# Kernel optimization log

Measured on AMD Instinct MI355X. Metric: run time of the kernel, lower is better.

Reference implementation:

```python
import jax, jax.numpy as jnp
import numpy as np

B, H, W, E = 8, 64, 64, 256  # channels == embedding (required by final Multiply)


def setup_inputs() -> dict:
    key = jax.random.key(0)
    k1, k2, k3 = jax.random.split(key, 3)
    inputs = jax.random.normal(k1, (B, H, W, E), dtype=jnp.float32)
    # Conv2D(embedding, 3, padding='same') params, HWIO layout
    conv_w = jax.random.normal(k2, (3, 3, E, E), dtype=jnp.float32) * (1.0 / np.sqrt(9 * E))
    conv_b = jnp.zeros((E,), dtype=jnp.float32)
    return {"inputs": inputs, "conv_w": conv_w, "conv_b": conv_b}


def reference(inputs, conv_w, conv_b):
    emb = conv_w.shape[-1]
    # conv1: 3x3 same-padded conv, NHWC
    x = jax.lax.conv_general_dilated(
        inputs, conv_w, window_strides=(1, 1), padding="SAME",
        dimension_numbers=("NHWC", "HWIO", "NHWC")) + conv_b
    b, h, w, e = x.shape
    x1 = x.reshape(b, h * w, e)                       # [B, N, E]
    scores = jnp.einsum("bne,bme->bnm", x1, x1)       # [B, N, N]
    attn = jax.nn.softmax(scores, axis=-1) / jnp.sqrt(jnp.asarray(emb, x.dtype))
    out = jnp.einsum("bnm,bme->bne", attn, x1)        # [B, N, E]
    # Original keras uses Reshape((inputs.shape[-2], inputs.shape[-3], -1)): (W, H, E)
    out = out.reshape(b, w, h, e)
    return out * inputs
```

## Files before the change

### kernel.cpp

```cpp
#include <hip/hip_runtime.h>
#include <hip/hip_bf16.h>

typedef __attribute__((ext_vector_type(4))) float f32x4;
typedef __attribute__((ext_vector_type(8))) _Float16 f16x8;
typedef unsigned short u16;

#define NB 8
#define NE 256
#define NN 4096
#define SD 64

__device__ __forceinline__ void gload_lds16(const void* g, void* l) {
  __builtin_amdgcn_global_load_lds((const __attribute__((address_space(1))) void*)g,
                                   (__attribute__((address_space(3))) void*)l, 16, 0, 0);
}
__device__ __forceinline__ float fexp2(float x) {
#if __has_builtin(__builtin_amdgcn_exp2f)
  return __builtin_amdgcn_exp2f(x);
#else
  return exp2f(x);
#endif
}

__global__ __launch_bounds__(256) void k_prep(const float* __restrict__ x, u16* __restrict__ outF,
                                              const float* __restrict__ w, u16* __restrict__ wT) {
  int bid = blockIdx.x;
  int tid = threadIdx.x;
  if (bid < 8192) {
    int i = bid * 256 + tid;
    float4 v = reinterpret_cast<const float4*>(x)[i];
    ushort4 o;
    o.x = __builtin_bit_cast(u16, (_Float16)v.x);
    o.y = __builtin_bit_cast(u16, (_Float16)v.y);
    o.z = __builtin_bit_cast(u16, (_Float16)v.z);
    o.w = __builtin_bit_cast(u16, (_Float16)v.w);
    reinterpret_cast<ushort4*>(outF)[i] = o;
  } else {
    int i = (bid - 8192) * 256 + tid;
    int t = i >> 16;
    int r = i & 65535;
    int ei = r >> 8, eo = r & 255;
    int o = (t << 16) + (eo << 8) + ei;
    wT[o] = __builtin_bit_cast(u16, (_Float16)w[i]);
  }
}

__global__ __launch_bounds__(256, 2) void k_conv(const u16* __restrict__ inF,
                                                 const u16* __restrict__ wT,
                                                 const float* __restrict__ bias,
                                                 u16* __restrict__ x1h) {
  __shared__ u16 Ahalo[264 * 64];
  __shared__ u16 BhL[2][128 * 64];
  int b = blockIdx.x >> 6;
  int rem = blockIdx.x & 63;
  int mt = rem >> 1, et = rem & 1;
  int h0 = mt << 1;
  int tid = threadIdx.x;
  int wid = tid >> 6, lane = tid & 63;
  int wr = wid >> 1, wc = wid & 1;
  int r = lane & 15, g = lane >> 4;
  f32x4 acc[4][4];
#pragma unroll
  for (int i = 0; i < 4; ++i)
#pragma unroll
    for (int j = 0; j < 4; ++j) acc[i][j] = (f32x4){0.f, 0.f, 0.f, 0.f};
  const long ibase = (long)b * NN * NE;

  const int bsw = ((((lane & 7) << 4) ^ (((lane >> 3) & 7) << 4)) >> 1);
  long bSrc[4];
#pragma unroll
  for (int i = 0; i < 4; ++i) {
    int c = wid * 4 + i;
    int eo = c * 8 + (lane >> 3);
    bSrc[i] = (long)(et * 128 + eo) * 256 + bsw;
  }
  int aHalo[9];
  const u16* aSrc[9];
#pragma unroll
  for (int j = 0; j < 9; ++j) {
    int c = wid + 4 * j;
    int slot = c * 8 + (lane >> 3);
    int hr = slot >= 198 ? 3 : (slot >= 132 ? 2 : (slot >= 66 ? 1 : 0));
    int hc = slot - hr * 66;
    int ir = h0 - 1 + hr, ic = hc - 1;
    aHalo[j] = ((unsigned)ir >= 64u) | ((unsigned)ic >= 64u);
    int irc = min(max(ir, 0), 63), icc = min(max(ic, 0), 63);
    int c8s = (lane & 7) ^ (slot & 7);
    aSrc[j] = inF + ibase + ((long)(irc * 64 + icc) << 8) + c8s * 8;
  }

#pragma unroll
  for (int i = 0; i < 4; ++i)
    gload_lds16(wT + bSrc[i], (char*)BhL[0] + (wid * 4 + i) * 1024);

#pragma unroll 1
  for (int kc = 0; kc < 4; ++kc) {
    __builtin_amdgcn_s_barrier();
#pragma unroll
    for (int j = 0; j < 9; ++j) {
      int c = wid + 4 * j;
      if (c < 33)
        gload_lds16(aSrc[j] + kc * 64, (char*)Ahalo + c * 1024);
    }
    asm volatile("s_waitcnt vmcnt(0)" ::: "memory");
#pragma unroll
    for (int j = 0; j < 9; ++j) {
      int c = wid + 4 * j;
      if (c < 33 && aHalo[j])
        *reinterpret_cast<float4*>((char*)Ahalo + c * 1024 + (lane << 4)) =
            make_float4(0.f, 0.f, 0.f, 0.f);
    }
    asm volatile("s_waitcnt lgkmcnt(0)" ::: "memory");
    __builtin_amdgcn_s_barrier();

#pragma unroll 1
    for (int t = 0; t < 9; ++t) {
      int gidx = kc * 9 + t;
      if (t > 0) {
        asm volatile("s_waitcnt vmcnt(0)" ::: "memory");
        __builtin_amdgcn_s_barrier();
      }
      if (gidx < 35) {
        int nt = t + 1 == 9 ? 0 : t + 1;
        int nkc = t + 1 == 9 ? kc + 1 : kc;
        long tkoff = ((long)nt << 16) + nkc * 64;
        char* dstB = (char*)BhL[(gidx + 1) & 1];
#pragma unroll
        for (int i = 0; i < 4; ++i)
          gload_lds16(wT + tkoff + bSrc[i], dstB + (wid * 4 + i) * 1024);
      }
      const u16* BB = BhL[gidx & 1];
      int dy = t / 3 - 1, dx = t % 3 - 1;
      int abase = (wr + 1 + dy) * 66 + 1 + dx;
#pragma unroll
      for (int ks = 0; ks < 2; ++ks) {
        int c8 = ks * 4 + g;
        f16x8 ah[4], bh[4];
#pragma unroll
        for (int mi = 0; mi < 4; ++mi) {
          int slot = abase + mi * 16 + r;
          int abyte = (slot << 7) + ((c8 << 4) ^ ((slot & 7) << 4));
          ah[mi] = *reinterpret_cast<const f16x8*>(reinterpret_cast<const char*>(Ahalo) + abyte);
        }
#pragma unroll
        for (int ni = 0; ni < 4; ++ni) {
          int col = wc * 64 + ni * 16 + r;
          int bbyte = (col << 7) + ((c8 << 4) ^ ((r & 7) << 4));
          bh[ni] = *reinterpret_cast<const f16x8*>(reinterpret_cast<const char*>(BB) + bbyte);
        }
#pragma unroll
        for (int mi = 0; mi < 4; ++mi)
#pragma unroll
          for (int ni = 0; ni < 4; ++ni)
            acc[mi][ni] = __builtin_amdgcn_mfma_f32_16x16x32_f16(ah[mi], bh[ni], acc[mi][ni], 0, 0, 0);
      }
    }
  }
#pragma unroll
  for (int mi = 0; mi < 4; ++mi)
#pragma unroll
    for (int ni = 0; ni < 4; ++ni) {
      int eo = et * 128 + wc * 64 + ni * 16 + r;
      float bz = bias[eo];
#pragma unroll
      for (int i = 0; i < 4; ++i) {
        int pix = mt * 128 + wr * 64 + mi * 16 + g * 4 + i;
        float v = acc[mi][ni][i] + bz;
        long o = ibase + (long)pix * NE + eo;
        x1h[o] = __builtin_bit_cast(u16, (_Float16)v);
      }
    }
}

__global__ __launch_bounds__(256) void k_trans(const u16* __restrict__ x1h, u16* __restrict__ x1T) {
  __shared__ u16 T[64][72];
  int bid = blockIdx.x;
  int b = bid >> 8, rem = bid & 255;
  int mt = rem >> 2, et = rem & 3;
  int tid = threadIdx.x;
  for (int c = tid; c < 512; c += 256) {
    int rr = c >> 3, c8 = c & 7;
    *reinterpret_cast<float4*>(&T[rr][c8 * 8]) =
        *reinterpret_cast<const float4*>(x1h + ((long)b * NN + mt * 64 + rr) * NE + et * 64 + c8 * 8);
  }
  __syncthreads();
  for (int c = tid; c < 512; c += 256) {
    int er = c >> 3, m8 = c & 7;
    union { u16 u[8]; float4 v; } p;
#pragma unroll
    for (int j = 0; j < 8; ++j) p.u[j] = T[m8 * 8 + j][er];
    *reinterpret_cast<float4*>(x1T + ((long)b * NE + et * 64 + er) * NN + mt * 64 + m8 * 8) = p.v;
  }
}

__global__ __launch_bounds__(256, 3) void k_flash7(const u16* __restrict__ x1h16,
                                                   const u16* __restrict__ x1T,
                                                   const float* __restrict__ inp,
                                                   float* __restrict__ out) {
  __shared__ char LDS[49152];
  int phys = blockIdx.x;
  int b = phys & 7;
  int qt = phys >> 3;
  int tid = threadIdx.x, wid = tid >> 6, lane = tid & 63;
  int l15 = lane & 15, g4 = (lane >> 4) & 3;
  const long bN = (long)b << 12;
  const long vtb = (long)b << 20;

  const long qrow = bN + qt * 64 + wid * 16 + l15;
  f16x8 qh[8];
#pragma unroll
  for (int kc = 0; kc < 8; ++kc) {
    qh[kc] = *reinterpret_cast<const f16x8*>(x1h16 + (qrow << 8) + kc * 32 + g4 * 8);
#pragma unroll
    for (int j = 0; j < 8; ++j)
      qh[kc][j] = (_Float16)((float)qh[kc][j] * 1.44269504f);
  }

  f32x4 o16[16];
#pragma unroll
  for (int et = 0; et < 16; ++et) o16[et] = (f32x4){0.f, 0.f, 0.f, 0.f};
  float mrow = -1.0e30f, lrow = 0.f;

  const u16* kS[4];
  const u16* vS[4];
  int off[4];
#pragma unroll
  for (int i = 0; i < 4; ++i) {
    int c = wid * 4 + i;
    off[i] = c << 10;
    int kr = c * 2 + (lane >> 5);
    int kcolb = ((lane & 31) << 4) ^ ((kr & 15) << 4);
    kS[i] = x1h16 + ((bN + kr) << 8) + (kcolb >> 1);
    int rp = c * 16 + (lane >> 2);
    int e = rp ^ ((rp >> 2) & 1);
    int vcolb = ((lane & 3) << 4) ^ ((e & 3) << 4);
    vS[i] = x1T + vtb + ((long)e << 12) + (vcolb >> 1);
  }

  const int vbase = ((l15 << 6) ^ ((l15 & 4) << 4)) + ((g4 * 16) ^ ((l15 & 3) << 4));
  const int kxor = l15 << 4;
  const int srcA = ((lane >> 4) & 1) * 32 + l15;
  const int srcB = srcA + 16;
  const bool hiHalf = (lane & 32) != 0;

#pragma unroll
  for (int i = 0; i < 4; ++i) { gload_lds16(kS[i], LDS + off[i]); kS[i] += 8192; }

#pragma unroll 1
  for (int it = 0; it < 128; ++it) {
    const char* KB = LDS + (it & 1) * 16384;
    char* VB = LDS + 32768;

    asm volatile("s_waitcnt vmcnt(0)" ::: "memory");
    __builtin_amdgcn_s_barrier();
    __builtin_amdgcn_sched_barrier(0);

    f32x4 st0 = (f32x4){0.f, 0.f, 0.f, 0.f}, st1 = st0;
    int krow0 = l15 << 9, krow1 = (16 + l15) << 9;
    __builtin_amdgcn_s_setprio(1);
#pragma unroll
    for (int kc = 0; kc < 8; ++kc) {
      int kb = (kc * 64 + g4 * 16) ^ kxor;
      f16x8 k0 = *reinterpret_cast<const f16x8*>(KB + krow0 + kb);
      f16x8 k1 = *reinterpret_cast<const f16x8*>(KB + krow1 + kb);
      st0 = __builtin_amdgcn_mfma_f32_16x16x32_f16(k0, qh[kc], st0, 0, 0, 0);
      st1 = __builtin_amdgcn_mfma_f32_16x16x32_f16(k1, qh[kc], st1, 0, 0, 0);
    }
    __builtin_amdgcn_s_setprio(0);

#pragma unroll
    for (int i = 0; i < 4; ++i) { gload_lds16(vS[i], VB + off[i]); vS[i] += 32; }
    if (it < 127) {
      char* KD = LDS + ((it + 1) & 1) * 16384;
#pragma unroll
      for (int i = 0; i < 4; ++i) { gload_lds16(kS[i], KD + off[i]); kS[i] += 8192; }
    }

    float tmax = fmaxf(fmaxf(fmaxf(st0[0], st0[1]), fmaxf(st0[2], st0[3])),
                       fmaxf(fmaxf(st1[0], st1[1]), fmaxf(st1[2], st1[3])));
    tmax = fmaxf(tmax, __shfl_xor(tmax, 16));
    tmax = fmaxf(tmax, __shfl_xor(tmax, 32));
    if (!__all(tmax <= mrow + 11.54f)) {
      float mnew = fmaxf(mrow, tmax);
      float alpha = fexp2(mrow - mnew);
      lrow *= alpha;
      float ar[4];
#pragma unroll
      for (int i = 0; i < 4; ++i) ar[i] = __shfl(alpha, g4 * 4 + i);
#pragma unroll
      for (int et = 0; et < 16; ++et)
#pragma unroll
        for (int i = 0; i < 4; ++i) o16[et][i] *= ar[i];
      mrow = mnew;
    }
#pragma unroll
    for (int i = 0; i < 4; ++i) { st0[i] = fexp2(st0[i] - mrow); st1[i] = fexp2(st1[i] - mrow); }
    float psum = (st0[0] + st0[1]) + (st0[2] + st0[3]) + (st1[0] + st1[1]) + (st1[2] + st1[3]);
    psum += __shfl_xor(psum, 16);
    psum += __shfl_xor(psum, 32);
    lrow += psum;

    int W0, W1, W2, W3;
    {
      unsigned a0 = __builtin_bit_cast(u16, (_Float16)st0[0]);
      unsigned a1 = __builtin_bit_cast(u16, (_Float16)st0[1]);
      unsigned a2 = __builtin_bit_cast(u16, (_Float16)st0[2]);
      unsigned a3 = __builtin_bit_cast(u16, (_Float16)st0[3]);
      unsigned b0 = __builtin_bit_cast(u16, (_Float16)st1[0]);
      unsigned b1 = __builtin_bit_cast(u16, (_Float16)st1[1]);
      unsigned b2 = __builtin_bit_cast(u16, (_Float16)st1[2]);
      unsigned b3 = __builtin_bit_cast(u16, (_Float16)st1[3]);
      W0 = (int)(a0 | (a1 << 16)); W1 = (int)(a2 | (a3 << 16));
      W2 = (int)(b0 | (b1 << 16)); W3 = (int)(b2 | (b3 << 16));
    }
    union PU { int w[4]; f16x8 v; } pa;
    {
      int u0a = __shfl(W0, srcA), u2a = __shfl(W2, srcA);
      int u1a = __shfl(W1, srcA), u3a = __shfl(W3, srcA);
      int u0b = __shfl(W0, srcB), u2b = __shfl(W2, srcB);
      int u1b = __shfl(W1, srcB), u3b = __shfl(W3, srcB);
      pa.w[0] = hiHalf ? u2a : u0a;
      pa.w[1] = hiHalf ? u3a : u1a;
      pa.w[2] = hiHalf ? u2b : u0b;
      pa.w[3] = hiHalf ? u3b : u1b;
    }

    if (it < 127) {
      asm volatile("s_waitcnt vmcnt(4)" ::: "memory");
    } else {
      asm volatile("s_waitcnt vmcnt(0)" ::: "memory");
    }
    __builtin_amdgcn_s_barrier();
    __builtin_amdgcn_sched_barrier(0);

    __builtin_amdgcn_s_setprio(1);
#pragma unroll
    for (int et = 0; et < 16; ++et) {
      f16x8 v = *reinterpret_cast<const f16x8*>(VB + vbase + et * 1024);
      o16[et] = __builtin_amdgcn_mfma_f32_16x16x32_f16(pa.v, v, o16[et], 0, 0, 0);
    }
    __builtin_amdgcn_s_setprio(0);
  }

  float linv = 1.0f / (16.0f * lrow);
  float lr[4];
#pragma unroll
  for (int i = 0; i < 4; ++i) lr[i] = __shfl(linv, g4 * 4 + i);
  const long ob = (bN + qt * 64 + wid * 16) << 8;
#pragma unroll
  for (int et = 0; et < 16; ++et)
#pragma unroll
    for (int i = 0; i < 4; ++i) {
      long off2 = ob + ((long)(g4 * 4 + i) << 8) + et * 16 + l15;
      out[off2] = o16[et][i] * lr[i] * inp[off2];
    }
}

extern "C" void kernel_launch(void* const* d_in, const int* in_sizes, int n_in,
                              void* d_out, int out_size, void* d_ws, size_t ws_size,
                              hipStream_t stream) {
  const float* inp   = (const float*)d_in[0];
  const float* convw = (const float*)d_in[1];
  const float* convb = (const float*)d_in[2];
  float* out = (float*)d_out;
  char* ws = (char*)d_ws;

  u16* x1h = (u16*)(ws);
  u16* x1T = (u16*)(ws + 16777216L);
  u16* inF = (u16*)(ws + 33554432L);
  u16* wT  = (u16*)(ws + 50331648L);

  k_prep<<<10496, 256, 0, stream>>>(inp, inF, convw, wT);
  k_conv<<<512, 256, 0, stream>>>(inF, wT, convb, x1h);
  k_trans<<<2048, 256, 0, stream>>>(x1h, x1T);
  k_flash7<<<512, 256, 0, stream>>>(x1h, x1T, inp, out);
}
```

Measured before the change: 287.6 us.

## Split attention KV range across two blocks and merge partials in separate kernel

The flash-attention kernel now splits each query tile's key/value sequence into two halves handled by separate blocks, doubling the grid from 512 to 1024. Each block writes unnormalized partial outputs plus its row max and row sum to workspace. A new merge kernel combines the halves with log-sum-exp rescaling, normalizes, and applies the final multiply by the inputs. The aim is better CU occupancy and more parallelism, at the cost of extra global traffic for the fp32 partials, an additional kernel launch, and a possible tail wave.

```diff
diff --git a/kernel.cpp b/kernel.cpp
--- a/kernel.cpp
+++ b/kernel.cpp
@@ -193,18 +193,20 @@
   }
 }
 
-__global__ __launch_bounds__(256, 3) void k_flash7(const u16* __restrict__ x1h16,
+__global__ __launch_bounds__(256, 3) void k_flash8(const u16* __restrict__ x1h16,
                                                    const u16* __restrict__ x1T,
-                                                   const float* __restrict__ inp,
-                                                   float* __restrict__ out) {
+                                                   float* __restrict__ Opart,
+                                                   float* __restrict__ ml) {
   __shared__ char LDS[49152];
   int phys = blockIdx.x;
   int b = phys & 7;
-  int qt = phys >> 3;
+  int half = (phys >> 3) & 1;
+  int qt = phys >> 4;
   int tid = threadIdx.x, wid = tid >> 6, lane = tid & 63;
   int l15 = lane & 15, g4 = (lane >> 4) & 3;
   const long bN = (long)b << 12;
   const long vtb = (long)b << 20;
+  const int kv0 = half << 11;
 
   const long qrow = bN + qt * 64 + wid * 16 + l15;
   f16x8 qh[8];
@@ -230,11 +232,11 @@
     off[i] = c << 10;
     int kr = c * 2 + (lane >> 5);
     int kcolb = ((lane & 31) << 4) ^ ((kr & 15) << 4);
-    kS[i] = x1h16 + ((bN + kr) << 8) + (kcolb >> 1);
+    kS[i] = x1h16 + ((bN + kv0 + kr) << 8) + (kcolb >> 1);
     int rp = c * 16 + (lane >> 2);
     int e = rp ^ ((rp >> 2) & 1);
     int vcolb = ((lane & 3) << 4) ^ ((e & 3) << 4);
-    vS[i] = x1T + vtb + ((long)e << 12) + (vcolb >> 1);
+    vS[i] = x1T + vtb + ((long)e << 12) + kv0 + (vcolb >> 1);
   }
 
   const int vbase = ((l15 << 6) ^ ((l15 & 4) << 4)) + ((g4 * 16) ^ ((l15 & 3) << 4));
@@ -247,7 +249,7 @@
   for (int i = 0; i < 4; ++i) { gload_lds16(kS[i], LDS + off[i]); kS[i] += 8192; }
 
 #pragma unroll 1
-  for (int it = 0; it < 128; ++it) {
+  for (int it = 0; it < 64; ++it) {
     const char* KB = LDS + (it & 1) * 16384;
     char* VB = LDS + 32768;
 
@@ -270,7 +272,7 @@
 
 #pragma unroll
     for (int i = 0; i < 4; ++i) { gload_lds16(vS[i], VB + off[i]); vS[i] += 32; }
-    if (it < 127) {
+    if (it < 63) {
       char* KD = LDS + ((it + 1) & 1) * 16384;
 #pragma unroll
       for (int i = 0; i < 4; ++i) { gload_lds16(kS[i], KD + off[i]); kS[i] += 8192; }
@@ -325,7 +327,7 @@
       pa.w[3] = hiHalf ? u3b : u1b;
     }
 
-    if (it < 127) {
+    if (it < 63) {
       asm volatile("s_waitcnt vmcnt(4)" ::: "memory");
     } else {
       asm volatile("s_waitcnt vmcnt(0)" ::: "memory");
@@ -342,18 +344,38 @@
     __builtin_amdgcn_s_setprio(0);
   }
 
-  float linv = 1.0f / (16.0f * lrow);
-  float lr[4];
-#pragma unroll
-  for (int i = 0; i < 4; ++i) lr[i] = __shfl(linv, g4 * 4 + i);
-  const long ob = (bN + qt * 64 + wid * 16) << 8;
+  const long grow0 = bN + qt * 64 + wid * 16;
+  float* Oh = Opart + (long)half * 8388608;
+  if (lane < 16) {
+    ml[half * 65536 + grow0 + l15] = mrow;
+    ml[half * 65536 + 32768 + grow0 + l15] = lrow;
+  }
 #pragma unroll
   for (int et = 0; et < 16; ++et)
 #pragma unroll
-    for (int i = 0; i < 4; ++i) {
-      long off2 = ob + ((long)(g4 * 4 + i) << 8) + et * 16 + l15;
-      out[off2] = o16[et][i] * lr[i] * inp[off2];
-    }
+    for (int i = 0; i < 4; ++i)
+      Oh[((grow0 + g4 * 4 + i) << 8) + et * 16 + l15] = o16[et][i];
+}
+
+__global__ __launch_bounds__(256) void k_merge(const float* __restrict__ O0, const float* __restrict__ O1,
+                                               const float* __restrict__ ml,
+                                               const float* __restrict__ inp, float* __restrict__ out) {
+  int g = blockIdx.x * 256 + threadIdx.x;
+  int row = g >> 6;
+  float m0 = ml[row], l0 = ml[32768 + row];
+  float m1 = ml[65536 + row], l1 = ml[98304 + row];
+  float M = fmaxf(m0, m1);
+  float f0 = fexp2(m0 - M), f1 = fexp2(m1 - M);
+  float s = 1.0f / (16.0f * (f0 * l0 + f1 * l1));
+  float4 a = reinterpret_cast<const float4*>(O0)[g];
+  float4 bb = reinterpret_cast<const float4*>(O1)[g];
+  float4 x = reinterpret_cast<const float4*>(inp)[g];
+  float4 o;
+  o.x = (f0 * a.x + f1 * bb.x) * s * x.x;
+  o.y = (f0 * a.y + f1 * bb.y) * s * x.y;
+  o.z = (f0 * a.z + f1 * bb.z) * s * x.z;
+  o.w = (f0 * a.w + f1 * bb.w) * s * x.w;
+  reinterpret_cast<float4*>(out)[g] = o;
 }
 
 extern "C" void kernel_launch(void* const* d_in, const int* in_sizes, int n_in,
@@ -365,13 +387,17 @@
   float* out = (float*)d_out;
   char* ws = (char*)d_ws;
 
-  u16* x1h = (u16*)(ws);
-  u16* x1T = (u16*)(ws + 16777216L);
-  u16* inF = (u16*)(ws + 33554432L);
-  u16* wT  = (u16*)(ws + 50331648L);
+  u16* x1h  = (u16*)(ws);
+  u16* x1T  = (u16*)(ws + 16777216L);
+  float* O0 = (float*)(ws + 33554432L);
+  float* O1 = (float*)(ws + 67108864L);
+  float* ml = (float*)(ws + 100663296L);
+  u16* inF  = (u16*)(ws + 33554432L);
+  u16* wT   = (u16*)(ws + 50331648L);
 
   k_prep<<<10496, 256, 0, stream>>>(inp, inF, convw, wT);
   k_conv<<<512, 256, 0, stream>>>(inF, wT, convb, x1h);
   k_trans<<<2048, 256, 0, stream>>>(x1h, x1T);
-  k_flash7<<<512, 256, 0, stream>>>(x1h, x1T, inp, out);
-}
+  k_flash8<<<1024, 256, 0, stream>>>(x1h, x1T, O0, ml);
+  k_merge<<<8192, 256, 0, stream>>>(O0, O1, ml, inp, out);
+}
```

New measurement: 314.8 us. +9.4%, slower.
